# Optimization experiments

Measured on AMD Instinct MI355X. Metric: run time of the kernel, lower is better.

Reference implementation:

```python
import jax, jax.numpy as jnp
import numpy as np
from jax import lax

B, C, P = 512, 1, 64
N_MEM = 32768
HID = 16


def _conv(x, w, b):
    # x: [B,Cin,H,W], w: [Cout,Cin,3,3]
    y = lax.conv_general_dilated(x, w, (1, 1), 'SAME',
                                 dimension_numbers=('NCHW', 'OIHW', 'NCHW'))
    return y + b[None, :, None, None]


def setup_inputs() -> dict:
    key = jax.random.key(0)
    ks = jax.random.split(key, 16)
    s = 0.05
    inp = {
        'noisy': jax.random.normal(ks[0], (B, C, P, P), jnp.float32),
        'mem_noise_bank': jax.random.normal(ks[1], (N_MEM, C, P, P), jnp.float32),
        'mem_clean_bank': jax.random.normal(ks[2], (N_MEM, C, P, P), jnp.float32),
        # frozen base denoiser (3-layer residual conv)
        'bw1': jax.random.normal(ks[3], (HID, C, 3, 3), jnp.float32) * s,
        'bb1': jnp.zeros((HID,), jnp.float32),
        'bw2': jax.random.normal(ks[4], (HID, HID, 3, 3), jnp.float32) * s,
        'bb2': jnp.zeros((HID,), jnp.float32),
        'bw3': jax.random.normal(ks[5], (C, HID, 3, 3), jnp.float32) * s,
        'bb3': jnp.zeros((C,), jnp.float32),
        # adapter convs (3*C -> HID -> HID -> C); torch zero-inits last conv,
        # we use small random weights so the output exercises the full path
        'aw1': jax.random.normal(ks[6], (HID, 3 * C, 3, 3), jnp.float32) * s,
        'ab1': jnp.zeros((HID,), jnp.float32),
        'aw2': jax.random.normal(ks[7], (HID, HID, 3, 3), jnp.float32) * s,
        'ab2': jnp.zeros((HID,), jnp.float32),
        'aw3': jax.random.normal(ks[8], (C, HID, 3, 3), jnp.float32) * s,
        'ab3': jnp.zeros((C,), jnp.float32),
    }
    return inp


def _base(noisy, bw1, bb1, bw2, bb2, bw3, bb3):
    h = jax.nn.relu(_conv(noisy, bw1, bb1))
    h = jax.nn.relu(_conv(h, bw2, bb2))
    return noisy - _conv(h, bw3, bb3)


def _select_memory(noisy, mem_noise_bank, mem_clean_bank):
    nf = noisy.reshape(B, -1)                  # [B, D]
    mf = mem_noise_bank.reshape(N_MEM, -1)     # [N, D]
    a2 = jnp.sum(nf * nf, axis=1, keepdims=True)   # [B,1]
    b2 = jnp.sum(mf * mf, axis=1)[None, :]         # [1,N]
    dists = a2 + b2 - 2.0 * (nf @ mf.T)            # [B,N]
    idx = jnp.argmin(dists, axis=1)                # [B]
    return mem_clean_bank[idx]                     # [B,C,P,P]


def reference(noisy, mem_noise_bank, mem_clean_bank,
              bw1, bb1, bw2, bb2, bw3, bb3,
              aw1, ab1, aw2, ab2, aw3, ab3):
    base_out = lax.stop_gradient(_base(noisy, bw1, bb1, bw2, bb2, bw3, bb3))
    mem_clean = lax.stop_gradient(
        _select_memory(noisy, mem_noise_bank, mem_clean_bank))
    x = jnp.concatenate([noisy, base_out, mem_clean], axis=1)  # [B,3C,P,P]
    h = jax.nn.relu(_conv(x, aw1, ab1))
    h = jax.nn.relu(_conv(h, aw2, ab2))
    delta = _conv(h, aw3, ab3)
    return base_out + delta
```

## Files before the change

### kernel.cpp

```cpp
#include <hip/hip_runtime.h>
#include <hip/hip_bf16.h>
#include <cstdint>

#define B_IMG 512
#define NMEM  32768
#define DD    4096
#define HID   16

typedef __attribute__((ext_vector_type(8))) short short8;
typedef __attribute__((ext_vector_type(4))) float f32x4;
typedef unsigned long long ull;

__device__ __forceinline__ void gload16(const void* g, const void* l) {
  __builtin_amdgcn_global_load_lds(
      (const __attribute__((address_space(1))) void*)g,
      (__attribute__((address_space(3))) void*)l, 16, 0, 0);
}

__device__ __forceinline__ ushort to_bf16u(float f) {
  uint32_t u = __float_as_uint(f);
  return (ushort)((u + 0x7fffu + ((u >> 16) & 1u)) >> 16);
}

__device__ __forceinline__ uint32_t cvtpk(float lo, float hi) {
  uint32_t r;
  asm("v_cvt_pk_bf16_f32 %0, %1, %2" : "=v"(r) : "v"(lo), "v"(hi));
  return r;
}

__global__ __launch_bounds__(256) void sqnorm_kernel(const float* __restrict__ x,
                                                     float* __restrict__ out) {
  const int row = blockIdx.x;
  const float4* p = reinterpret_cast<const float4*>(x + (size_t)row * DD);
  float s = 0.f;
#pragma unroll
  for (int j = 0; j < 4; ++j) {
    float4 v = p[threadIdx.x + 256 * j];
    s += v.x * v.x + v.y * v.y + v.z * v.z + v.w * v.w;
  }
#pragma unroll
  for (int o = 32; o > 0; o >>= 1) s += __shfl_down(s, o);
  __shared__ float ls[4];
  if ((threadIdx.x & 63) == 0) ls[threadIdx.x >> 6] = s;
  __syncthreads();
  if (threadIdx.x == 0) out[row] = (ls[0] + ls[1]) + (ls[2] + ls[3]);
}

__global__ __launch_bounds__(256) void split_hi_kernel(const float* __restrict__ x,
                                                       ushort* __restrict__ hi,
                                                       float* __restrict__ nrm) {
  const int row = blockIdx.x;
  const int t = threadIdx.x;
  const float4* p = reinterpret_cast<const float4*>(x + (size_t)row * DD);
  ushort4* ph = reinterpret_cast<ushort4*>(hi + (size_t)row * DD);
  float s = 0.f;
#pragma unroll
  for (int j = 0; j < 4; ++j) {
    float4 v = p[t + 256 * j];
    float vv[4] = {v.x, v.y, v.z, v.w};
    ushort4 h;
    ushort* hp = &h.x;
#pragma unroll
    for (int q = 0; q < 4; ++q) {
      float f = vv[q];
      s += f * f;
      hp[q] = to_bf16u(f);
    }
    ph[t + 256 * j] = h;
  }
#pragma unroll
  for (int o = 32; o > 0; o >>= 1) s += __shfl_down(s, o);
  __shared__ float ls[4];
  if ((t & 63) == 0) ls[t >> 6] = s;
  __syncthreads();
  if (t == 0) nrm[row] = (ls[0] + ls[1]) + (ls[2] + ls[3]);
}

__global__ __launch_bounds__(256) void dist1f_kernel(
    const ushort* __restrict__ Ah_g, const float* __restrict__ Bf,
    const float* __restrict__ a2, float* __restrict__ dists) {
  const int d = blockIdx.x;
  const int xcd = d & 7;
  const int rest = d >> 3;
  const int mb = rest & 3;
  const int nb = (rest >> 2) * 8 + xcd;
  const int m0 = mb * 128;
  const int n0 = nb * 128;

  __shared__ __align__(16) char la[8192];
  __shared__ __align__(16) char lbB[8192];
  __shared__ float b2loc[128];

  const int t = threadIdx.x;
  const int lane = t & 63;
  const int wid = t >> 6;
  const int wm = wid >> 1;
  const int wn = wid & 1;

  f32x4 acc[4][4];
#pragma unroll
  for (int mi = 0; mi < 4; ++mi)
#pragma unroll
    for (int ni = 0; ni < 4; ++ni) {
      f32x4 z = {0.f, 0.f, 0.f, 0.f};
      acc[mi][ni] = z;
    }

  const int r0 = t >> 2, g0 = t & 3;
  const int c0 = ((g0 ^ ((r0 >> 1) & 3)) << 3);
  const int r1 = 64 + r0;
  const int c1 = ((g0 ^ ((r1 >> 1) & 3)) << 3);
  const float* Bp0 = Bf + (size_t)(n0 + r0) * DD + c0;
  const float* Bp1 = Bf + (size_t)(n0 + r1) * DD + c1;
  float s0 = 0.f, s1 = 0.f;

  for (int k0 = 0; k0 < DD; k0 += 32) {
#pragma unroll
    for (int j = 0; j < 2; ++j) {
      const int e = (j * 256 + t) * 8;
      const int row = e >> 5;
      const int gpos = (e >> 3) & 3;
      const int col = ((gpos ^ ((row >> 1) & 3)) << 3);
      gload16(Ah_g + ((size_t)(m0 + row) * DD + k0 + col), la + e * 2);
    }
    float4 f00 = *(const float4*)(Bp0 + k0);
    float4 f01 = *(const float4*)(Bp0 + k0 + 4);
    float4 f10 = *(const float4*)(Bp1 + k0);
    float4 f11 = *(const float4*)(Bp1 + k0 + 4);
    s0 += f00.x * f00.x + f00.y * f00.y + f00.z * f00.z + f00.w * f00.w;
    s0 += f01.x * f01.x + f01.y * f01.y + f01.z * f01.z + f01.w * f01.w;
    s1 += f10.x * f10.x + f10.y * f10.y + f10.z * f10.z + f10.w * f10.w;
    s1 += f11.x * f11.x + f11.y * f11.y + f11.z * f11.z + f11.w * f11.w;
    uint4 p0, p1;
    p0.x = cvtpk(f00.x, f00.y); p0.y = cvtpk(f00.z, f00.w);
    p0.z = cvtpk(f01.x, f01.y); p0.w = cvtpk(f01.z, f01.w);
    p1.x = cvtpk(f10.x, f10.y); p1.y = cvtpk(f10.z, f10.w);
    p1.z = cvtpk(f11.x, f11.y); p1.w = cvtpk(f11.z, f11.w);
    *(uint4*)(lbB + t * 16) = p0;
    *(uint4*)(lbB + 4096 + t * 16) = p1;
    __syncthreads();

    short8 ah[4];
#pragma unroll
    for (int mi = 0; mi < 4; ++mi) {
      const int r = wm * 64 + mi * 16 + (lane & 15);
      const int off = r * 64 + ((((lane >> 4) ^ (r >> 1)) & 3) << 4);
      ah[mi] = *(const short8*)(la + off);
    }
#pragma unroll
    for (int ni = 0; ni < 4; ++ni) {
      const int r = wn * 64 + ni * 16 + (lane & 15);
      const int off = r * 64 + ((((lane >> 4) ^ (r >> 1)) & 3) << 4);
      short8 bh = *(const short8*)(lbB + off);
#pragma unroll
      for (int mi = 0; mi < 4; ++mi)
        acc[mi][ni] = __builtin_amdgcn_mfma_f32_16x16x32_bf16(ah[mi], bh, acc[mi][ni], 0, 0, 0);
    }
    __syncthreads();
  }

  s0 += __shfl_xor(s0, 1); s0 += __shfl_xor(s0, 2);
  s1 += __shfl_xor(s1, 1); s1 += __shfl_xor(s1, 2);
  if ((t & 3) == 0) { b2loc[r0] = s0; b2loc[r1] = s1; }
  __syncthreads();

#pragma unroll
  for (int mi = 0; mi < 4; ++mi)
#pragma unroll
    for (int j = 0; j < 4; ++j) {
      const int m = m0 + wm * 64 + mi * 16 + (lane >> 4) * 4 + j;
      const float a2v = a2[m];
#pragma unroll
      for (int ni = 0; ni < 4; ++ni) {
        const int nl = wn * 64 + ni * 16 + (lane & 15);
        dists[(size_t)m * NMEM + n0 + nl] = (a2v + b2loc[nl]) - 2.0f * acc[mi][ni][j];
      }
    }
}

#define MARGIN 4.0f
#define MAXC 64
#define NCH 4
#define CHW (NMEM / NCH)
__global__ __launch_bounds__(256) void refine_kernel(
    const float* __restrict__ dists, const float* __restrict__ A,
    const float* __restrict__ Bm, const float* __restrict__ a2,
    ull* __restrict__ best) {
  const int m = blockIdx.x;
  const int base = blockIdx.y * CHW;
  const int t = threadIdx.x;
  const int lane = t & 63, wid = t >> 6;
  const float4* r4 = reinterpret_cast<const float4*>(dists + (size_t)m * NMEM + base);

  float lmin = 3.4e38f;
  for (int i = t; i < CHW / 4; i += 256) {
    float4 v = r4[i];
    lmin = fminf(lmin, fminf(fminf(v.x, v.y), fminf(v.z, v.w)));
  }
#pragma unroll
  for (int o = 32; o > 0; o >>= 1) lmin = fminf(lmin, __shfl_down(lmin, o));
  __shared__ float ws4[4];
  __shared__ float red[4];
  __shared__ float red2[4];
  __shared__ int cnt;
  __shared__ int cand[MAXC];
  if (lane == 0) ws4[wid] = lmin;
  if (t == 0) cnt = 0;
  __syncthreads();
  const float thresh = fminf(fminf(ws4[0], ws4[1]), fminf(ws4[2], ws4[3])) + MARGIN;

  for (int i = t; i < CHW / 4; i += 256) {
    float4 v = r4[i];
    float vv[4] = {v.x, v.y, v.z, v.w};
#pragma unroll
    for (int q = 0; q < 4; ++q)
      if (vv[q] < thresh) {
        int c = atomicAdd(&cnt, 1);
        if (c < MAXC) cand[c] = base + i * 4 + q;
      }
  }
  __syncthreads();
  const int nc = min(cnt, MAXC);

  ull bkey = ~0ull;
  const float4* a4 = reinterpret_cast<const float4*>(A + (size_t)m * DD);
  for (int c = 0; c < nc; ++c) {
    const int n = cand[c];
    const float4* b4 = reinterpret_cast<const float4*>(Bm + (size_t)n * DD);
    float s = 0.f, s2 = 0.f;
    for (int i = t; i < DD / 4; i += 256) {
      float4 av = a4[i], bv = b4[i];
      s += av.x * bv.x + av.y * bv.y + av.z * bv.z + av.w * bv.w;
      s2 += bv.x * bv.x + bv.y * bv.y + bv.z * bv.z + bv.w * bv.w;
    }
#pragma unroll
    for (int o = 32; o > 0; o >>= 1) {
      s += __shfl_down(s, o);
      s2 += __shfl_down(s2, o);
    }
    if (lane == 0) { red[wid] = s; red2[wid] = s2; }
    __syncthreads();
    if (t == 0) {
      const float dot = (red[0] + red[1]) + (red[2] + red[3]);
      const float b2n = (red2[0] + red2[1]) + (red2[2] + red2[3]);
      const float dv = (a2[m] + b2n) - 2.0f * dot;
      const ull key = ((ull)__float_as_uint(dv) << 32) | (unsigned)n;
      if (key < bkey) bkey = key;
    }
    __syncthreads();
  }
  if (t == 0) atomicMin(&best[m], bkey);
}

__global__ __launch_bounds__(256) void dist_argmin_kernel(
    const float* __restrict__ A, const float* __restrict__ Bm,
    const float* __restrict__ a2, const float* __restrict__ b2,
    ull* __restrict__ best) {
  __shared__ float As[32][128];
  __shared__ float Bs[32][128];
  const int tid = threadIdx.x;
  const int m0 = blockIdx.y * 128;
  const int n0 = blockIdx.x * 128;
  const int tm = tid >> 4, tn = tid & 15;
  const int sr = tid >> 3;
  const int sc = (tid & 7) << 2;
  float acc[8][8];
#pragma unroll
  for (int i = 0; i < 8; ++i)
#pragma unroll
    for (int j = 0; j < 8; ++j) acc[i][j] = 0.f;
  for (int k0 = 0; k0 < DD; k0 += 32) {
    __syncthreads();
#pragma unroll
    for (int r = 0; r < 4; ++r) {
      const int row = sr + (r << 5);
      float4 va = *reinterpret_cast<const float4*>(&A[(size_t)(m0 + row) * DD + k0 + sc]);
      As[sc + 0][row] = va.x; As[sc + 1][row] = va.y;
      As[sc + 2][row] = va.z; As[sc + 3][row] = va.w;
      float4 vb = *reinterpret_cast<const float4*>(&Bm[(size_t)(n0 + row) * DD + k0 + sc]);
      Bs[sc + 0][row] = vb.x; Bs[sc + 1][row] = vb.y;
      Bs[sc + 2][row] = vb.z; Bs[sc + 3][row] = vb.w;
    }
    __syncthreads();
#pragma unroll 8
    for (int kk = 0; kk < 32; ++kk) {
      float4 a0 = *reinterpret_cast<const float4*>(&As[kk][tm * 8]);
      float4 a1 = *reinterpret_cast<const float4*>(&As[kk][tm * 8 + 4]);
      float4 b0 = *reinterpret_cast<const float4*>(&Bs[kk][tn * 8]);
      float4 b1 = *reinterpret_cast<const float4*>(&Bs[kk][tn * 8 + 4]);
      float a[8] = {a0.x, a0.y, a0.z, a0.w, a1.x, a1.y, a1.z, a1.w};
      float b[8] = {b0.x, b0.y, b0.z, b0.w, b1.x, b1.y, b1.z, b1.w};
#pragma unroll
      for (int i = 0; i < 8; ++i)
#pragma unroll
        for (int j = 0; j < 8; ++j) acc[i][j] += a[i] * b[j];
    }
  }
  __syncthreads();
  ull* red = reinterpret_cast<ull*>(&As[0][0]);
#pragma unroll
  for (int i = 0; i < 8; ++i) {
    const int m = m0 + tm * 8 + i;
    const float a2v = a2[m];
    float bd = 3.4e38f;
    int bn = 0;
#pragma unroll
    for (int j = 0; j < 8; ++j) {
      const int n = n0 + tn * 8 + j;
      const float dval = (a2v + b2[n]) - 2.0f * acc[i][j];
      if (dval < bd) { bd = dval; bn = n; }
    }
    red[(tm * 8 + i) * 16 + tn] = ((ull)__float_as_uint(bd) << 32) | (unsigned)bn;
  }
  __syncthreads();
  if (tid < 128) {
    ull k = red[tid * 16];
#pragma unroll
    for (int t2 = 1; t2 < 16; ++t2) {
      ull c = red[tid * 16 + t2];
      if (c < k) k = c;
    }
    atomicMin(&best[m0 + tid], k);
  }
}

__global__ __launch_bounds__(256) void wprep_kernel(
    const float* __restrict__ w1, const float* __restrict__ w2,
    const float* __restrict__ w3, int ncin,
    float* __restrict__ wt1, ushort* __restrict__ wh2, ushort* __restrict__ wl2,
    ushort* __restrict__ wh3, ushort* __restrict__ wl3) {
  const int i = blockIdx.x * 256 + threadIdx.x;
  const int n1 = ncin * 144;
  if (i < n1) {
    const int co = i & 15, r = i >> 4;
    const int ci = r / 9, kk = r % 9;
    wt1[(ci * 9 + kk) * 16 + co] = w1[(co * ncin + ci) * 9 + kk];
  } else if (i < n1 + 5120) {
    const int j = i - n1;
    const int which = j / 2560;
    const int jj = j % 2560;
    const int co = jj / 160, k = jj % 160;
    float f = 0.f;
    if (which == 0) {
      if (k < 144) f = w2[co * 144 + (k & 15) * 9 + (k >> 4)];
    } else {
      if (co == 0 && k < 144) f = w3[(k & 15) * 9 + (k >> 4)];
    }
    const ushort hb = to_bf16u(f);
    const float fl = f - __uint_as_float((uint32_t)hb << 16);
    ushort* dh = (which == 0) ? wh2 : wh3;
    ushort* dl = (which == 0) ? wl2 : wl3;
    dh[co * 160 + k] = hb;
    dl[co * 160 + k] = to_bf16u(fl);
  }
}

template <int NCIN>
__global__ __launch_bounds__(256, 4) void fused_conv3_kernel(
    const float* __restrict__ chan0, const float* __restrict__ chan1,
    const float* __restrict__ memC, const ull* __restrict__ best,
    const float* __restrict__ wt1, const float* __restrict__ b1v,
    const ushort* __restrict__ wh2, const ushort* __restrict__ wl2,
    const float* __restrict__ b2v,
    const ushort* __restrict__ wh3, const ushort* __restrict__ wl3,
    const float* __restrict__ b3v,
    const float* __restrict__ addend, float sign, float* __restrict__ outp) {
  constexpr int SIN_SZ = NCIN * 1600;
  constexpr int H1 = SIN_SZ;
  constexpr int H2 = H1 + 10368;
  constexpr int ZP = H2 + 10368;
  constexpr int W1 = ZP + 64;
  constexpr int SB = W1 + NCIN * 576;
  __shared__ __align__(16) char smem[SB + 128];
  float* sIn = (float*)smem;
  float* sW1 = (float*)(smem + W1);
  float* sB = (float*)(smem + SB);

  const int tid = threadIdx.x;
  const int lane = tid & 63, wid = tid >> 6;
  const int img = blockIdx.x / 25;
  const int t = blockIdx.x % 25;
  const int y0 = (t / 5) * 14, x0 = (t % 5) * 14;

  const float* cptr[NCIN];
  cptr[0] = chan0 + (size_t)img * DD;
  if (NCIN == 3) {
    cptr[1] = chan1 + (size_t)img * DD;
    cptr[2] = memC + (size_t)(unsigned)(best[img] & 0xffffffffull) * DD;
  }

  if (tid < 16) *(float*)(smem + ZP + tid * 4) = 0.f;
  for (int i = tid; i < NCIN * 144; i += 256) sW1[i] = wt1[i];
  if (tid < 16) sB[tid] = b1v[tid];
  else if (tid < 32) sB[tid] = b2v[tid - 16];
  for (int i = tid; i < NCIN * 400; i += 256) {
    const int ci = i / 400, r = i % 400, yy = r / 20, xx = r % 20;
    const int gy = y0 + yy - 3, gx = x0 + xx - 3;
    float v = 0.f;
    if (gy >= 0 && gy < 64 && gx >= 0 && gx < 64) v = cptr[ci][gy * 64 + gx];
    sIn[ci * 400 + yy * 20 + xx] = v;
  }
  __syncthreads();

  {
    const int p0 = tid;
    const int p1t = tid + 256;
    const bool has1 = (p1t < 324);
    const int p1 = has1 ? p1t : 0;
    const int y0p = p0 / 18, x0p = p0 % 18;
    const int y1p = p1 / 18, x1p = p1 % 18;
    const int gy0 = y0 + y0p - 2, gx0 = x0 + x0p - 2;
    const int gy1 = y0 + y1p - 2, gx1 = x0 + x1p - 2;
    const bool in0 = ((unsigned)gy0 < 64u) && ((unsigned)gx0 < 64u);
    const bool in1 = has1 && ((unsigned)gy1 < 64u) && ((unsigned)gx1 < 64u);

    float acc0[16], acc1[16];
#pragma unroll
    for (int co = 0; co < 16; ++co) {
      acc0[co] = sB[co];
      acc1[co] = sB[co];
    }
    int io0 = y0p * 20 + x0p;
    int io1 = y1p * 20 + x1p;
    int wo = 0;
    int dx = 0, dy = 0;
#pragma unroll 1
    for (int tk = 0; tk < NCIN * 9; ++tk) {
      const float v0 = sIn[io0];
      const float v1 = sIn[io1];
      const float4* wq = reinterpret_cast<const float4*>(sW1 + wo);
#pragma unroll
      for (int q = 0; q < 4; ++q) {
        float4 w = wq[q];
        acc0[4 * q + 0] += w.x * v0; acc1[4 * q + 0] += w.x * v1;
        acc0[4 * q + 1] += w.y * v0; acc1[4 * q + 1] += w.y * v1;
        acc0[4 * q + 2] += w.z * v0; acc1[4 * q + 2] += w.z * v1;
        acc0[4 * q + 3] += w.w * v0; acc1[4 * q + 3] += w.w * v1;
      }
      wo += 16;
      if (++dx == 3) {
        dx = 0;
        if (++dy == 3) { dy = 0; io0 += 358; io1 += 358; }
        else { io0 += 18; io1 += 18; }
      } else { io0 += 1; io1 += 1; }
    }
    short8 h0, h1v;
#pragma unroll
    for (int c = 0; c < 8; ++c) {
      h0[c] = (short)(in0 ? to_bf16u(fmaxf(acc0[c], 0.f)) : 0);
      h1v[c] = (short)(in0 ? to_bf16u(fmaxf(acc0[8 + c], 0.f)) : 0);
    }
    *(short8*)(smem + H1 + p0 * 16) = h0;
    *(short8*)(smem + H1 + 5184 + p0 * 16) = h1v;
    if (has1) {
#pragma unroll
      for (int c = 0; c < 8; ++c) {
        h0[c] = (short)(in1 ? to_bf16u(fmaxf(acc1[c], 0.f)) : 0);
        h1v[c] = (short)(in1 ? to_bf16u(fmaxf(acc1[8 + c], 0.f)) : 0);
      }
      *(short8*)(smem + H1 + p1 * 16) = h0;
      *(short8*)(smem + H1 + 5184 + p1 * 16) = h1v;
    }
  }
  __syncthreads();

  const int xn = lane & 15;
  const int xk = lane >> 4;
  f32x4 acc2[4];
#pragma unroll
  for (int g = 0; g < 4; ++g) { f32x4 z = {0.f, 0.f, 0.f, 0.f}; acc2[g] = z; }
#pragma unroll
  for (int kq = 0; kq < 5; ++kq) {
    const int k0 = kq * 32;
    const int we = xn * 160 + k0 + xk * 8;
    short8 ah = *(const short8*)(wh2 + we);
    short8 al = *(const short8*)(wl2 + we);
    const int kb = k0 + xk * 8;
    const int tap = kb >> 4, cih = (kb >> 3) & 1;
    const bool zp = (tap >= 9);
    const int dy = tap / 3, dx = tap % 3;
    const int bbase = H1 + cih * 5184 + ((dy * 18) + xn + dx) * 16;
#pragma unroll
    for (int g = 0; g < 4; ++g) {
      const int y = wid * 4 + g;
      const int boff = zp ? ZP : (bbase + y * 288);
      short8 b = *(const short8*)(smem + boff);
      acc2[g] = __builtin_amdgcn_mfma_f32_16x16x32_bf16(ah, b, acc2[g], 0, 0, 0);
      acc2[g] = __builtin_amdgcn_mfma_f32_16x16x32_bf16(al, b, acc2[g], 0, 0, 0);
    }
  }
#pragma unroll
  for (int g = 0; g < 4; ++g) {
    const int y = wid * 4 + g;
    const int gy = y0 + y - 1, gx = x0 + xn - 1;
    const bool inimg = ((unsigned)gy < 64u) && ((unsigned)gx < 64u);
#pragma unroll
    for (int j = 0; j < 4; ++j) {
      const int co = xk * 4 + j;
      const float v = inimg ? fmaxf(acc2[g][j] + sB[16 + co], 0.f) : 0.f;
      *(ushort*)(smem + H2 + (co >> 3) * 5184 + (y * 18 + xn) * 16 + (co & 7) * 2) =
          to_bf16u(v);
    }
  }
  __syncthreads();

  f32x4 acc3[4];
#pragma unroll
  for (int g = 0; g < 4; ++g) { f32x4 z = {0.f, 0.f, 0.f, 0.f}; acc3[g] = z; }
#pragma unroll
  for (int kq = 0; kq < 5; ++kq) {
    const int k0 = kq * 32;
    const int we = xn * 160 + k0 + xk * 8;
    short8 ah = *(const short8*)(wh3 + we);
    short8 al = *(const short8*)(wl3 + we);
    const int kb = k0 + xk * 8;
    const int tap = kb >> 4, cih = (kb >> 3) & 1;
    const bool zp = (tap >= 9);
    const int dy = tap / 3, dx = tap % 3;
    const int bbase = H2 + cih * 5184 + ((dy * 18) + xn + dx) * 16;
#pragma unroll
    for (int g = 0; g < 4; ++g) {
      const int y = wid * 4 + g;
      const int boff = zp ? ZP : (bbase + y * 288);
      short8 b = *(const short8*)(smem + boff);
      acc3[g] = __builtin_amdgcn_mfma_f32_16x16x32_bf16(ah, b, acc3[g], 0, 0, 0);
      acc3[g] = __builtin_amdgcn_mfma_f32_16x16x32_bf16(al, b, acc3[g], 0, 0, 0);
    }
  }
  if (xk == 0) {
#pragma unroll
    for (int g = 0; g < 4; ++g) {
      const int y = wid * 4 + g;
      const int gy = y0 + y, gx = x0 + xn;
      if (y < 14 && xn < 14 && gy < 64 && gx < 64) {
        const size_t o = (size_t)img * DD + gy * 64 + gx;
        outp[o] = addend[o] + sign * (acc3[g][0] + b3v[0]);
      }
    }
  }
}

extern "C" void kernel_launch(void* const* d_in, const int* in_sizes, int n_in,
                              void* d_out, int out_size, void* d_ws, size_t ws_size,
                              hipStream_t stream) {
  (void)in_sizes; (void)n_in; (void)out_size;
  const float* noisy = (const float*)d_in[0];
  const float* memN  = (const float*)d_in[1];
  const float* memC  = (const float*)d_in[2];
  const float* bw1 = (const float*)d_in[3];
  const float* bb1 = (const float*)d_in[4];
  const float* bw2 = (const float*)d_in[5];
  const float* bb2 = (const float*)d_in[6];
  const float* bw3 = (const float*)d_in[7];
  const float* bb3 = (const float*)d_in[8];
  const float* aw1 = (const float*)d_in[9];
  const float* ab1 = (const float*)d_in[10];
  const float* aw2 = (const float*)d_in[11];
  const float* ab2 = (const float*)d_in[12];
  const float* aw3 = (const float*)d_in[13];
  const float* ab3 = (const float*)d_in[14];
  float* out_f32 = (float*)d_out;

  char* ws = (char*)d_ws;
  size_t off = 0;
  auto take = [&](size_t bytes) -> char* {
    char* p = ws + off;
    off += (bytes + 255) & ~(size_t)255;
    return p;
  };
  float* b2 = (float*)take((size_t)NMEM * 4);
  float* a2 = (float*)take((size_t)B_IMG * 4);
  ull* best = (ull*)take((size_t)B_IMG * 8);
  float* base_out = (float*)take((size_t)B_IMG * DD * 4);
  float* wt1b = (float*)take(144 * 4);
  ushort* wh2b = (ushort*)take(2560 * 2);
  ushort* wl2b = (ushort*)take(2560 * 2);
  ushort* wh3b = (ushort*)take(2560 * 2);
  ushort* wl3b = (ushort*)take(2560 * 2);
  float* wt1a = (float*)take(432 * 4);
  ushort* wh2a = (ushort*)take(2560 * 2);
  ushort* wl2a = (ushort*)take(2560 * 2);
  ushort* wh3a = (ushort*)take(2560 * 2);
  ushort* wl3a = (ushort*)take(2560 * 2);
  const size_t off_common = off;

  ushort* Ah = (ushort*)take((size_t)B_IMG * DD * 2);
  float* dists = (float*)take((size_t)B_IMG * NMEM * 4);
  const bool use_mfma = (off + 1024) <= ws_size;
  if (!use_mfma) off = off_common;

  wprep_kernel<<<21, 256, 0, stream>>>(bw1, bw2, bw3, 1, wt1b, wh2b, wl2b, wh3b, wl3b);
  wprep_kernel<<<22, 256, 0, stream>>>(aw1, aw2, aw3, 3, wt1a, wh2a, wl2a, wh3a, wl3a);

  hipMemsetAsync(best, 0xFF, (size_t)B_IMG * 8, stream);
  if (use_mfma) {
    split_hi_kernel<<<B_IMG, 256, 0, stream>>>(noisy, Ah, a2);
    dist1f_kernel<<<(NMEM / 128) * (B_IMG / 128), 256, 0, stream>>>(
        Ah, memN, a2, dists);
    refine_kernel<<<dim3(B_IMG, NCH), 256, 0, stream>>>(dists, noisy, memN, a2, best);
  } else {
    sqnorm_kernel<<<NMEM, 256, 0, stream>>>(memN, b2);
    sqnorm_kernel<<<B_IMG, 256, 0, stream>>>(noisy, a2);
    dist_argmin_kernel<<<dim3(NMEM / 128, B_IMG / 128), 256, 0, stream>>>(
        noisy, memN, a2, b2, best);
  }

  fused_conv3_kernel<1><<<B_IMG * 25, 256, 0, stream>>>(
      noisy, nullptr, nullptr, nullptr,
      wt1b, bb1, wh2b, wl2b, bb2, wh3b, wl3b, bb3, noisy, -1.0f, base_out);
  fused_conv3_kernel<3><<<B_IMG * 25, 256, 0, stream>>>(
      noisy, base_out, memC, best,
      wt1a, ab1, wh2a, wl2a, ab2, wh3a, wl3a, ab3, base_out, 1.0f, out_f32);
}
```

Measured before the change: 591.7 us.

## Double-buffer LDS tiles in distance GEMM to overlap loads with MFMA

Doubles the A and B LDS staging buffers in the distance GEMM kernel and prefetches the next K-slice while MFMAs run on the current one. The bank fp32 loads, norm accumulation and bf16 conversion for the next tile move after the MFMA block, and one of the two barriers per iteration is removed. The aim is to hide global memory latency behind compute. The cost is more LDS per block (about 32KB), which may reduce occupancy, plus more registers held live across the MFMA section.

```diff
diff --git a/kernel.cpp b/kernel.cpp
--- a/kernel.cpp
+++ b/kernel.cpp
@@ -87,8 +87,8 @@
   const int m0 = mb * 128;
   const int n0 = nb * 128;
 
-  __shared__ __align__(16) char la[8192];
-  __shared__ __align__(16) char lbB[8192];
+  __shared__ __align__(16) char la[2][8192];
+  __shared__ __align__(16) char lbB[2][8192];
   __shared__ float b2loc[128];
 
   const int t = threadIdx.x;
@@ -114,19 +114,24 @@
   const float* Bp1 = Bf + (size_t)(n0 + r1) * DD + c1;
   float s0 = 0.f, s1 = 0.f;
 
-  for (int k0 = 0; k0 < DD; k0 += 32) {
-#pragma unroll
-    for (int j = 0; j < 2; ++j) {
-      const int e = (j * 256 + t) * 8;
-      const int row = e >> 5;
-      const int gpos = (e >> 3) & 3;
-      const int col = ((gpos ^ ((row >> 1) & 3)) << 3);
-      gload16(Ah_g + ((size_t)(m0 + row) * DD + k0 + col), la + e * 2);
-    }
-    float4 f00 = *(const float4*)(Bp0 + k0);
-    float4 f01 = *(const float4*)(Bp0 + k0 + 4);
-    float4 f10 = *(const float4*)(Bp1 + k0);
-    float4 f11 = *(const float4*)(Bp1 + k0 + 4);
+  int arow[2], acol[2];
+#pragma unroll
+  for (int j = 0; j < 2; ++j) {
+    const int e = (j * 256 + t) * 8;
+    arow[j] = e >> 5;
+    const int gpos = (e >> 3) & 3;
+    acol[j] = ((gpos ^ ((arow[j] >> 1) & 3)) << 3);
+  }
+
+  {
+#pragma unroll
+    for (int j = 0; j < 2; ++j)
+      gload16(Ah_g + ((size_t)(m0 + arow[j]) * DD + acol[j]),
+              la[0] + (j * 256 + t) * 16);
+    float4 f00 = *(const float4*)(Bp0);
+    float4 f01 = *(const float4*)(Bp0 + 4);
+    float4 f10 = *(const float4*)(Bp1);
+    float4 f11 = *(const float4*)(Bp1 + 4);
     s0 += f00.x * f00.x + f00.y * f00.y + f00.z * f00.z + f00.w * f00.w;
     s0 += f01.x * f01.x + f01.y * f01.y + f01.z * f01.z + f01.w * f01.w;
     s1 += f10.x * f10.x + f10.y * f10.y + f10.z * f10.z + f10.w * f10.w;
@@ -136,27 +141,59 @@
     p0.z = cvtpk(f01.x, f01.y); p0.w = cvtpk(f01.z, f01.w);
     p1.x = cvtpk(f10.x, f10.y); p1.y = cvtpk(f10.z, f10.w);
     p1.z = cvtpk(f11.x, f11.y); p1.w = cvtpk(f11.z, f11.w);
-    *(uint4*)(lbB + t * 16) = p0;
-    *(uint4*)(lbB + 4096 + t * 16) = p1;
-    __syncthreads();
+    *(uint4*)(lbB[0] + t * 16) = p0;
+    *(uint4*)(lbB[0] + 4096 + t * 16) = p1;
+  }
+  __syncthreads();
+
+  int cur = 0;
+  for (int k0 = 0; k0 < DD; k0 += 32) {
+    const int nxt = cur ^ 1;
+    const bool more = (k0 + 32) < DD;
+    float4 f00, f01, f10, f11;
+    if (more) {
+      f00 = *(const float4*)(Bp0 + k0 + 32);
+      f01 = *(const float4*)(Bp0 + k0 + 36);
+      f10 = *(const float4*)(Bp1 + k0 + 32);
+      f11 = *(const float4*)(Bp1 + k0 + 36);
+#pragma unroll
+      for (int j = 0; j < 2; ++j)
+        gload16(Ah_g + ((size_t)(m0 + arow[j]) * DD + k0 + 32 + acol[j]),
+                la[nxt] + (j * 256 + t) * 16);
+    }
 
     short8 ah[4];
 #pragma unroll
     for (int mi = 0; mi < 4; ++mi) {
       const int r = wm * 64 + mi * 16 + (lane & 15);
       const int off = r * 64 + ((((lane >> 4) ^ (r >> 1)) & 3) << 4);
-      ah[mi] = *(const short8*)(la + off);
+      ah[mi] = *(const short8*)(la[cur] + off);
     }
 #pragma unroll
     for (int ni = 0; ni < 4; ++ni) {
       const int r = wn * 64 + ni * 16 + (lane & 15);
       const int off = r * 64 + ((((lane >> 4) ^ (r >> 1)) & 3) << 4);
-      short8 bh = *(const short8*)(lbB + off);
+      short8 bh = *(const short8*)(lbB[cur] + off);
 #pragma unroll
       for (int mi = 0; mi < 4; ++mi)
         acc[mi][ni] = __builtin_amdgcn_mfma_f32_16x16x32_bf16(ah[mi], bh, acc[mi][ni], 0, 0, 0);
     }
+
+    if (more) {
+      s0 += f00.x * f00.x + f00.y * f00.y + f00.z * f00.z + f00.w * f00.w;
+      s0 += f01.x * f01.x + f01.y * f01.y + f01.z * f01.z + f01.w * f01.w;
+      s1 += f10.x * f10.x + f10.y * f10.y + f10.z * f10.z + f10.w * f10.w;
+      s1 += f11.x * f11.x + f11.y * f11.y + f11.z * f11.z + f11.w * f11.w;
+      uint4 p0, p1;
+      p0.x = cvtpk(f00.x, f00.y); p0.y = cvtpk(f00.z, f00.w);
+      p0.z = cvtpk(f01.x, f01.y); p0.w = cvtpk(f01.z, f01.w);
+      p1.x = cvtpk(f10.x, f10.y); p1.y = cvtpk(f10.z, f10.w);
+      p1.z = cvtpk(f11.x, f11.y); p1.w = cvtpk(f11.z, f11.w);
+      *(uint4*)(lbB[nxt] + t * 16) = p0;
+      *(uint4*)(lbB[nxt] + 4096 + t * 16) = p1;
+    }
     __syncthreads();
+    cur = nxt;
   }
 
   s0 += __shfl_xor(s0, 1); s0 += __shfl_xor(s0, 2);
```

Result: slower. 660.1 us (+11.6%).
